# Kernel optimization log

Hardware: AMD Instinct MI355X
Metric: run time of the kernel (lower is better)

## Reference

```python
import jax, jax.numpy as jnp
import numpy as np

N_NODES = 100000
N_EDGES = 3200000
IN_FEAT = 512
HIDDEN = 16
N_CLASSES = 40


def gcn_conv(x, W, b, row, col, n):
    """PyG-style GCNConv: linear transform, add self-loops, symmetric deg^-1/2
    normalization, gather-scatter aggregation, bias."""
    self_idx = jnp.arange(n, dtype=row.dtype)
    row_sl = jnp.concatenate([row, self_idx])  # [E + N]
    col_sl = jnp.concatenate([col, self_idx])
    deg = jax.ops.segment_sum(jnp.ones_like(row_sl, dtype=x.dtype), row_sl, num_segments=n)
    dinv = jnp.where(deg > 0, jax.lax.rsqrt(deg), 0.0)
    norm = dinv[row_sl] * dinv[col_sl]  # [E + N]
    h = x @ W  # [n, out] -- transform first (cheap since out dim is small)
    msg = h[col_sl] * norm[:, None]  # gather + scale
    out = jax.ops.segment_sum(msg, row_sl, num_segments=n)  # scatter-add
    return out + b


def setup_inputs() -> dict:
    key = jax.random.key(0)
    k1, k2, k3, k4, k5 = jax.random.split(key, 5)
    x = jax.random.normal(k1, (N_NODES, IN_FEAT), dtype=jnp.float32)
    edge_index = jax.random.randint(k2, (2, N_EDGES), 0, N_NODES, dtype=jnp.int64)
    # Glorot-style init for linear weights
    W1 = jax.random.normal(k3, (IN_FEAT, HIDDEN), dtype=jnp.float32) / np.sqrt(IN_FEAT)
    b1 = jnp.zeros((HIDDEN,), dtype=jnp.float32)
    W2 = jax.random.normal(k4, (HIDDEN, N_CLASSES), dtype=jnp.float32) / np.sqrt(HIDDEN)
    b2 = jnp.zeros((N_CLASSES,), dtype=jnp.float32)
    return {"x": x, "edge_index": edge_index, "W1": W1, "b1": b1, "W2": W2, "b2": b2}


def reference(x, edge_index, W1, b1, W2, b2):
    row, col = edge_index[0], edge_index[1]
    n = x.shape[0]
    h = jax.nn.relu(gcn_conv(x, W1, b1, row, col, n))
    # dropout is identity at inference (training=False)
    out = gcn_conv(h, W2, b2, row, col, n)
    return jax.nn.log_softmax(out, axis=1)
```

## Files before the change

### kernel.cpp

```cpp
#include <hip/hip_runtime.h>

#define NFEAT 512
#define HID 16
#define NCLS 40
#define BROWS 256
#define BCAP 16384

typedef unsigned int uint32;
typedef float f4 __attribute__((ext_vector_type(4)));

__device__ __forceinline__ uint32 f2bf(float f) {
    uint32 u = __float_as_uint(f);
    return (u + 0x7FFFu + ((u >> 16) & 1u)) >> 16;
}
__device__ __forceinline__ float bf2f(uint32 h) {
    return __uint_as_float(h << 16);
}

__global__ void k_zero(int* __restrict__ p, int m) {
    int i = blockIdx.x * blockDim.x + threadIdx.x;
    if (i < m) p[i] = 0;
}

__global__ __launch_bounds__(256) void k_pairs(const int* __restrict__ row,
                                               const int* __restrict__ col,
                                               int* __restrict__ bcur,
                                               uint32* __restrict__ pairs, int E, int nb) {
    __shared__ int lhist[512];
    __shared__ int lbase[512];
    int chunk = (E + gridDim.x - 1) / gridDim.x;
    int s = blockIdx.x * chunk;
    int e = min(s + chunk, E);
    for (int b = threadIdx.x; b < nb; b += 256) lhist[b] = 0;
    __syncthreads();
    for (int i = s + threadIdx.x; i < e; i += 256)
        atomicAdd(&lhist[row[i] >> 8], 1);
    __syncthreads();
    for (int b = threadIdx.x; b < nb; b += 256) {
        int h = lhist[b];
        lbase[b] = h ? atomicAdd(&bcur[b], h) : 0;
        lhist[b] = 0;
    }
    __syncthreads();
    for (int i = s + threadIdx.x; i < e; i += 256) {
        int r = row[i], c = col[i];
        int b = r >> 8;
        int off = lbase[b] + atomicAdd(&lhist[b], 1);
        if (off < BCAP)
            pairs[(size_t)b * BCAP + off] = ((uint32)(r & 255) << 17) | (uint32)c;
    }
}

__global__ __launch_bounds__(256) void k_deg(const int* __restrict__ bcur,
                                             const uint32* __restrict__ pairs,
                                             int* __restrict__ cnt,
                                             float* __restrict__ dinv, int n) {
    __shared__ int lh[BROWS];
    int b = blockIdx.x;
    int bo = b * BCAP;
    int c2 = min(bcur[b], BCAP);
    lh[threadIdx.x] = 0;
    __syncthreads();
    for (int p = bo + (int)threadIdx.x; p < bo + c2; p += 256)
        atomicAdd(&lh[pairs[p] >> 17], 1);
    __syncthreads();
    int i = b * BROWS + threadIdx.x;
    if (i < n) {
        int c = lh[threadIdx.x];
        cnt[i] = c;
        dinv[i] = rsqrtf((float)c + 1.0f);
    }
}

__global__ __launch_bounds__(256, 4) void k_fused(const int* __restrict__ bcur,
                                                  const uint32* __restrict__ pairs,
                                                  const int* __restrict__ cnt,
                                                  int* __restrict__ csr,
                                                  int* __restrict__ start,
                                                  int* __restrict__ end,
                                                  const float* __restrict__ x,
                                                  const float* __restrict__ W,
                                                  const float* __restrict__ dinv,
                                                  uint32* __restrict__ g1,
                                                  int n, int nbCsr) {
    __shared__ float smem[8704];
    const int tid = threadIdx.x;

    if (blockIdx.x < (uint32)nbCsr) {
        int* sm   = (int*)smem;
        int* lcur = (int*)smem + 256;
        int b = blockIdx.x;
        int base = b * BROWS;
        int i = base + tid;
        int bo = b * BCAP;
        int cntb = min(bcur[b], BCAP);
        int e2 = bo + cntb;

        int c = (i < n) ? cnt[i] : 0;
        sm[tid] = c;
        __syncthreads();
        for (int off = 1; off < 256; off <<= 1) {
            int t = (tid >= off) ? sm[tid - off] : 0;
            __syncthreads();
            sm[tid] += t;
            __syncthreads();
        }
        int excl = sm[tid] - c;
        lcur[tid] = excl;
        if (i < n) {
            start[i] = bo + excl;
            end[i]   = bo + excl + c;
        }
        __syncthreads();
        for (int p = bo + tid; p < e2; p += 256) {
            uint32 pk = pairs[p];
            int off = atomicAdd(&lcur[pk >> 17], 1);
            csr[bo + off] = (int)(pk & 0x1FFFFu);
        }
        return;
    }

    float* Wl = smem;
    const int ks = tid & 7;
    const int g  = tid >> 3;

#pragma unroll
    for (int i = 0; i < 8; i++) {
        int fidx = tid + i * 256;
        int k = fidx >> 2, j4 = fidx & 3;
        float4 v = reinterpret_cast<const float4*>(W)[fidx];
        *reinterpret_cast<float4*>(&Wl[k * 16 + (k >> 2) * 4 + j4 * 4]) = v;
    }
    __syncthreads();

    const int rbase = (blockIdx.x - nbCsr) * 64 + g * 2;
    const int r0 = min(rbase, n - 1);
    const int r1 = min(rbase + 1, n - 1);
    const f4* xq0 = reinterpret_cast<const f4*>(x + (size_t)r0 * NFEAT);
    const f4* xq1 = reinterpret_cast<const f4*>(x + (size_t)r1 * NFEAT);

    float acc[2][16];
#pragma unroll
    for (int rr = 0; rr < 2; rr++)
#pragma unroll
        for (int j = 0; j < 16; j++) acc[rr][j] = 0.f;

    f4 xv[2], xn[2];
    xv[0] = __builtin_nontemporal_load(&xq0[ks]);
    xv[1] = __builtin_nontemporal_load(&xq1[ks]);

    for (int c = 0; c < 16; c++) {
        if (c < 15) {
            xn[0] = __builtin_nontemporal_load(&xq0[(c + 1) * 8 + ks]);
            xn[1] = __builtin_nontemporal_load(&xq1[(c + 1) * 8 + ks]);
        }
#pragma unroll
        for (int m = 0; m < 4; m++) {
            int k = c * 32 + ks * 4 + m;
            const float* wrow = &Wl[k * 16 + (k >> 2) * 4];
            float4 wv[4];
#pragma unroll
            for (int j4 = 0; j4 < 4; j4++)
                wv[j4] = *reinterpret_cast<const float4*>(wrow + j4 * 4);
#pragma unroll
            for (int rr = 0; rr < 2; rr++) {
                float xs = xv[rr][m];
#pragma unroll
                for (int j4 = 0; j4 < 4; j4++) {
                    acc[rr][j4 * 4 + 0] = fmaf(xs, wv[j4].x, acc[rr][j4 * 4 + 0]);
                    acc[rr][j4 * 4 + 1] = fmaf(xs, wv[j4].y, acc[rr][j4 * 4 + 1]);
                    acc[rr][j4 * 4 + 2] = fmaf(xs, wv[j4].z, acc[rr][j4 * 4 + 2]);
                    acc[rr][j4 * 4 + 3] = fmaf(xs, wv[j4].w, acc[rr][j4 * 4 + 3]);
                }
            }
        }
        xv[0] = xn[0];
        xv[1] = xn[1];
    }

#pragma unroll
    for (int off = 1; off < 8; off <<= 1)
#pragma unroll
        for (int rr = 0; rr < 2; rr++)
#pragma unroll
            for (int j = 0; j < 16; j++)
                acc[rr][j] += __shfl_xor(acc[rr][j], off, 8);

    if (ks == 0) {
#pragma unroll
        for (int rr = 0; rr < 2; rr++) {
            int r = rbase + rr;
            if (r < n) {
                float dr = dinv[r];
                uint32 us[8];
#pragma unroll
                for (int q = 0; q < 8; q++) {
                    uint32 lo = f2bf(dr * acc[rr][q * 2]);
                    uint32 hi = f2bf(dr * acc[rr][q * 2 + 1]);
                    us[q] = lo | (hi << 16);
                }
                uint4* o = reinterpret_cast<uint4*>(g1 + (size_t)r * 8);
                o[0] = make_uint4(us[0], us[1], us[2], us[3]);
                o[1] = make_uint4(us[4], us[5], us[6], us[7]);
            }
        }
    }
}

__global__ __launch_bounds__(256) void k_agg1(const uint32* __restrict__ g1,
                                              const int* __restrict__ start,
                                              const int* __restrict__ end,
                                              const int* __restrict__ csr,
                                              const float* __restrict__ dinv,
                                              const float* __restrict__ b1,
                                              uint32* __restrict__ g2, int n) {
    int g = threadIdx.x >> 3;
    int l = threadIdx.x & 7;
    int r = blockIdx.x * 32 + g;
    if (r >= n) return;
    int s = start[r], e = end[r];
    float a0 = 0.f, a1 = 0.f;
    int p = s;
    for (; p + 8 <= e; p += 8) {
        int c[8];
#pragma unroll
        for (int u = 0; u < 8; u++) c[u] = csr[p + u];
        uint32 hv[8];
#pragma unroll
        for (int u = 0; u < 8; u++) hv[u] = g1[c[u] * 8 + l];
#pragma unroll
        for (int u = 0; u < 8; u++) {
            a0 += bf2f(hv[u] & 0xFFFFu);
            a1 += bf2f(hv[u] >> 16);
        }
    }
    for (; p < e; p++) {
        uint32 h = g1[csr[p] * 8 + l];
        a0 += bf2f(h & 0xFFFFu);
        a1 += bf2f(h >> 16);
    }
    uint32 hs = g1[r * 8 + l];
    float dr = dinv[r];
    float z0 = fmaf(dr, a0 + bf2f(hs & 0xFFFFu), b1[2 * l]);
    float z1 = fmaf(dr, a1 + bf2f(hs >> 16), b1[2 * l + 1]);
    g2[r * 8 + l] = f2bf(dr * fmaxf(z0, 0.f)) | (f2bf(dr * fmaxf(z1, 0.f)) << 16);
}

__global__ __launch_bounds__(256) void k_agg2(const uint32* __restrict__ g2,
                                              const int* __restrict__ start,
                                              const int* __restrict__ end,
                                              const int* __restrict__ csr,
                                              const float* __restrict__ dinv,
                                              const float* __restrict__ W2,
                                              const float* __restrict__ b2,
                                              float* __restrict__ out, int n) {
    __shared__ float vsm[32][17];
    int g = threadIdx.x >> 3;
    int l = threadIdx.x & 7;
    int r = blockIdx.x * 32 + g;
    float a0 = 0.f, a1 = 0.f;
    if (r < n) {
        int s = start[r], e = end[r];
        int p = s;
        for (; p + 8 <= e; p += 8) {
            int c[8];
#pragma unroll
            for (int u = 0; u < 8; u++) c[u] = csr[p + u];
            uint32 hv[8];
#pragma unroll
            for (int u = 0; u < 8; u++) hv[u] = g2[c[u] * 8 + l];
#pragma unroll
            for (int u = 0; u < 8; u++) {
                a0 += bf2f(hv[u] & 0xFFFFu);
                a1 += bf2f(hv[u] >> 16);
            }
        }
        for (; p < e; p++) {
            uint32 h = g2[csr[p] * 8 + l];
            a0 += bf2f(h & 0xFFFFu);
            a1 += bf2f(h >> 16);
        }
        uint32 hs = g2[r * 8 + l];
        float dr = dinv[r];
        a0 = dr * (a0 + bf2f(hs & 0xFFFFu));
        a1 = dr * (a1 + bf2f(hs >> 16));
    }
    vsm[g][2 * l] = a0;
    vsm[g][2 * l + 1] = a1;
    __syncthreads();
    if (r >= n) return;

    float vloc[16];
#pragma unroll
    for (int k = 0; k < 16; k++) vloc[k] = vsm[g][k];

    float z[5];
#pragma unroll
    for (int i = 0; i < 5; i++) z[i] = b2[l + 8 * i];
#pragma unroll
    for (int k = 0; k < 16; k++) {
        float vk = vloc[k];
        const float* wk = W2 + k * NCLS;
#pragma unroll
        for (int i = 0; i < 5; i++) z[i] = fmaf(vk, wk[l + 8 * i], z[i]);
    }
    float m = z[0];
#pragma unroll
    for (int i = 1; i < 5; i++) m = fmaxf(m, z[i]);
#pragma unroll
    for (int off = 1; off < 8; off <<= 1) m = fmaxf(m, __shfl_xor(m, off, 8));
    float ssum = 0.f;
#pragma unroll
    for (int i = 0; i < 5; i++) ssum += __expf(z[i] - m);
#pragma unroll
    for (int off = 1; off < 8; off <<= 1) ssum += __shfl_xor(ssum, off, 8);
    float ls = m + logf(ssum);
    float* o = out + (size_t)r * NCLS;
#pragma unroll
    for (int i = 0; i < 5; i++) o[l + 8 * i] = z[i] - ls;
}


extern "C" void kernel_launch(void* const* d_in, const int* in_sizes, int n_in,
                              void* d_out, int out_size, void* d_ws, size_t ws_size,
                              hipStream_t stream) {
    const float* x  = (const float*)d_in[0];
    const int*   ei = (const int*)d_in[1];
    const float* W1 = (const float*)d_in[2];
    const float* b1 = (const float*)d_in[3];
    const float* W2 = (const float*)d_in[4];
    const float* b2 = (const float*)d_in[5];

    const int n = in_sizes[0] / NFEAT;
    const int E = in_sizes[1] / 2;
    const int* row = ei;
    const int* col = ei + E;
    const int nb = (n + BROWS - 1) / BROWS;

    char* w = (char*)d_ws;
    auto alloc = [&](size_t bytes) {
        void* p = (void*)w;
        w += (bytes + 255) & ~(size_t)255;
        return p;
    };
    int*    start = (int*)alloc((size_t)n * 4);
    int*    end   = (int*)alloc((size_t)n * 4);
    int*    cnt   = (int*)alloc((size_t)n * 4);
    int*    bcur  = (int*)alloc(2048);
    float*  dinv  = (float*)alloc((size_t)n * 4);
    int*    csr   = (int*)alloc((size_t)nb * BCAP * 4);
    uint32* pairs = (uint32*)alloc((size_t)nb * BCAP * 4);
    uint32* g1    = (uint32*)alloc((size_t)n * HID * 2);
    uint32* g2    = (uint32*)alloc((size_t)n * HID * 2);

    k_zero<<<1, 512, 0, stream>>>(bcur, nb);
    k_pairs<<<512, 256, 0, stream>>>(row, col, bcur, pairs, E, nb);
    k_deg<<<nb, 256, 0, stream>>>(bcur, pairs, cnt, dinv, n);
    k_fused<<<nb + (n + 63) / 64, 256, 0, stream>>>(bcur, pairs, cnt, csr, start, end,
                                                    x, W1, dinv, g1, n, nb);
    k_agg1<<<(n + 31) / 32, 256, 0, stream>>>(g1, start, end, csr, dinv, b1, g2, n);
    k_agg2<<<(n + 31) / 32, 256, 0, stream>>>(g2, start, end, csr, dinv, W2, b2,
                                              (float*)d_out, n);
}
```

Measured before the change: 186.3 us.

## Vectorize edge loads in pair binning, deepen x prefetch, unroll aggregation gathers by 16

```diff
diff --git a/kernel.cpp b/kernel.cpp
--- a/kernel.cpp
+++ b/kernel.cpp
@@ -28,13 +28,26 @@
                                                uint32* __restrict__ pairs, int E, int nb) {
     __shared__ int lhist[512];
     __shared__ int lbase[512];
-    int chunk = (E + gridDim.x - 1) / gridDim.x;
-    int s = blockIdx.x * chunk;
-    int e = min(s + chunk, E);
+    const int E4 = E >> 2;
+    const int chunk4 = (E4 + gridDim.x - 1) / gridDim.x;
+    const int s4 = blockIdx.x * chunk4;
+    const int e4 = min(s4 + chunk4, E4);
+    const int4* rp = reinterpret_cast<const int4*>(row);
+    const int4* cp = reinterpret_cast<const int4*>(col);
+
     for (int b = threadIdx.x; b < nb; b += 256) lhist[b] = 0;
     __syncthreads();
-    for (int i = s + threadIdx.x; i < e; i += 256)
-        atomicAdd(&lhist[row[i] >> 8], 1);
+    for (int i4 = s4 + (int)threadIdx.x; i4 < e4; i4 += 256) {
+        int4 r4 = rp[i4];
+        atomicAdd(&lhist[r4.x >> 8], 1);
+        atomicAdd(&lhist[r4.y >> 8], 1);
+        atomicAdd(&lhist[r4.z >> 8], 1);
+        atomicAdd(&lhist[r4.w >> 8], 1);
+    }
+    if (blockIdx.x == gridDim.x - 1) {
+        for (int i = E4 * 4 + (int)threadIdx.x; i < E; i += 256)
+            atomicAdd(&lhist[row[i] >> 8], 1);
+    }
     __syncthreads();
     for (int b = threadIdx.x; b < nb; b += 256) {
         int h = lhist[b];
@@ -42,12 +55,26 @@
         lhist[b] = 0;
     }
     __syncthreads();
-    for (int i = s + threadIdx.x; i < e; i += 256) {
-        int r = row[i], c = col[i];
-        int b = r >> 8;
-        int off = lbase[b] + atomicAdd(&lhist[b], 1);
-        if (off < BCAP)
-            pairs[(size_t)b * BCAP + off] = ((uint32)(r & 255) << 17) | (uint32)c;
+    for (int i4 = s4 + (int)threadIdx.x; i4 < e4; i4 += 256) {
+        int4 r4 = rp[i4];
+        int4 c4 = cp[i4];
+#pragma unroll
+        for (int u = 0; u < 4; u++) {
+            int r = (&r4.x)[u], c = (&c4.x)[u];
+            int b = r >> 8;
+            int off = lbase[b] + atomicAdd(&lhist[b], 1);
+            if (off < BCAP)
+                pairs[(size_t)b * BCAP + off] = ((uint32)(r & 255) << 17) | (uint32)c;
+        }
+    }
+    if (blockIdx.x == gridDim.x - 1) {
+        for (int i = E4 * 4 + (int)threadIdx.x; i < E; i += 256) {
+            int r = row[i], c = col[i];
+            int b = r >> 8;
+            int off = lbase[b] + atomicAdd(&lhist[b], 1);
+            if (off < BCAP)
+                pairs[(size_t)b * BCAP + off] = ((uint32)(r & 255) << 17) | (uint32)c;
+        }
     }
 }
 
@@ -145,14 +172,16 @@
 #pragma unroll
         for (int j = 0; j < 16; j++) acc[rr][j] = 0.f;
 
-    f4 xv[2], xn[2];
-    xv[0] = __builtin_nontemporal_load(&xq0[ks]);
-    xv[1] = __builtin_nontemporal_load(&xq1[ks]);
+    f4 xv[2], xn1[2], xn2[2];
+    xv[0]  = __builtin_nontemporal_load(&xq0[ks]);
+    xv[1]  = __builtin_nontemporal_load(&xq1[ks]);
+    xn1[0] = __builtin_nontemporal_load(&xq0[8 + ks]);
+    xn1[1] = __builtin_nontemporal_load(&xq1[8 + ks]);
 
     for (int c = 0; c < 16; c++) {
-        if (c < 15) {
-            xn[0] = __builtin_nontemporal_load(&xq0[(c + 1) * 8 + ks]);
-            xn[1] = __builtin_nontemporal_load(&xq1[(c + 1) * 8 + ks]);
+        if (c < 14) {
+            xn2[0] = __builtin_nontemporal_load(&xq0[(c + 2) * 8 + ks]);
+            xn2[1] = __builtin_nontemporal_load(&xq1[(c + 2) * 8 + ks]);
         }
 #pragma unroll
         for (int m = 0; m < 4; m++) {
@@ -174,8 +203,10 @@
                 }
             }
         }
-        xv[0] = xn[0];
-        xv[1] = xn[1];
+        xv[0] = xn1[0];
+        xv[1] = xn1[1];
+        xn1[0] = xn2[0];
+        xn1[1] = xn2[1];
     }
 
 #pragma unroll
@@ -221,6 +252,19 @@
     int s = start[r], e = end[r];
     float a0 = 0.f, a1 = 0.f;
     int p = s;
+    for (; p + 16 <= e; p += 16) {
+        int c[16];
+#pragma unroll
+        for (int u = 0; u < 16; u++) c[u] = csr[p + u];
+        uint32 hv[16];
+#pragma unroll
+        for (int u = 0; u < 16; u++) hv[u] = g1[c[u] * 8 + l];
+#pragma unroll
+        for (int u = 0; u < 16; u++) {
+            a0 += bf2f(hv[u] & 0xFFFFu);
+            a1 += bf2f(hv[u] >> 16);
+        }
+    }
     for (; p + 8 <= e; p += 8) {
         int c[8];
 #pragma unroll
@@ -262,6 +306,19 @@
     if (r < n) {
         int s = start[r], e = end[r];
         int p = s;
+        for (; p + 16 <= e; p += 16) {
+            int c[16];
+#pragma unroll
+            for (int u = 0; u < 16; u++) c[u] = csr[p + u];
+            uint32 hv[16];
+#pragma unroll
+            for (int u = 0; u < 16; u++) hv[u] = g2[c[u] * 8 + l];
+#pragma unroll
+            for (int u = 0; u < 16; u++) {
+                a0 += bf2f(hv[u] & 0xFFFFu);
+                a1 += bf2f(hv[u] >> 16);
+            }
+        }
         for (; p + 8 <= e; p += 8) {
             int c[8];
 #pragma unroll
```

After: 176.1 us. 5.5% less time.
